# Kernel tuning notes

Hardware: AMD Instinct MI355X
Metric: run time of the kernel (lower is better)

Reference implementation:

```python
import jax, jax.numpy as jnp
import numpy as np

N = 50000      # nodes
E = 800000     # edges (avg degree 16)
IN = 512       # in_feats
HID = 64       # hidden_dim
HEADS = 4      # num_heads
NC = 40        # num_classes


def setup_inputs() -> dict:
    key = jax.random.key(0)
    ks = jax.random.split(key, 12)

    def p(k, shape, fan_in):
        return jax.random.normal(k, shape, jnp.float32) * (1.0 / np.sqrt(fan_in))

    x = jax.random.normal(ks[0], (N, IN), jnp.float32)
    edge_index = jax.random.randint(ks[1], (2, E), 0, N)
    return dict(
        x=x,
        edge_index=edge_index,
        W1=p(ks[2], (IN, HEADS * HID), IN),
        att_src1=p(ks[3], (HEADS, HID), HID),
        att_dst1=p(ks[4], (HEADS, HID), HID),
        b1=jnp.zeros((HEADS * HID,), jnp.float32),
        W2=p(ks[5], (HEADS * HID, HID), HEADS * HID),
        att_src2=p(ks[6], (1, HID), HID),
        att_dst2=p(ks[7], (1, HID), HID),
        b2=jnp.zeros((HID,), jnp.float32),
        mw1=p(ks[8], (HID, 64), HID),
        mb1=jnp.zeros((64,), jnp.float32),
        mw2=p(ks[9], (64, NC), 64),
        mb2=jnp.zeros((NC,), jnp.float32),
    )


def gat_layer(x, edge_index, W, att_src, att_dst, bias):
    # PyG GATConv with add_self_loops=False, concat=True, negative_slope=0.2
    H, C = att_src.shape
    n = x.shape[0]
    h = (x @ W).reshape(n, H, C)                       # [N,H,C]
    a_src = jnp.sum(h * att_src, axis=-1)              # [N,H]
    a_dst = jnp.sum(h * att_dst, axis=-1)              # [N,H]
    src, dst = edge_index[0], edge_index[1]
    e = jax.nn.leaky_relu(a_src[src] + a_dst[dst], 0.2)  # [E,H]
    # segment softmax grouped by destination node
    m = jax.ops.segment_max(e, dst, num_segments=n)
    ex = jnp.exp(e - m[dst])
    denom = jax.ops.segment_sum(ex, dst, num_segments=n)
    alpha = ex / (denom[dst] + 1e-16)                  # [E,H]
    out = jax.ops.segment_sum(h[src] * alpha[:, :, None], dst, num_segments=n)  # [N,H,C]
    return out.reshape(n, H * C) + bias


def reference(x, edge_index, W1, att_src1, att_dst1, b1,
              W2, att_src2, att_dst2, b2, mw1, mb1, mw2, mb2):
    h = jax.nn.elu(gat_layer(x, edge_index, W1, att_src1, att_dst1, b1))   # [N, HEADS*HID]
    emb = gat_layer(h, edge_index, W2, att_src2, att_dst2, b2)             # [N, HID] (heads=1)
    return jax.nn.relu(emb @ mw1 + mb1) @ mw2 + mb2                        # [N, NC]
```

## Files before the change

### kernel.cpp

```cpp
#include <hip/hip_runtime.h>

#define N_NODES 50000
#define N_EDGES 800000
#define SCAN_B 196

typedef short bf16x8 __attribute__((ext_vector_type(8)));
typedef float f32x4 __attribute__((ext_vector_type(4)));

__device__ __forceinline__ unsigned short f2bf_rne(float x) {
  unsigned u = __float_as_uint(x);
  u += 0x7FFFu + ((u >> 16) & 1u);
  return (unsigned short)(u >> 16);
}

__global__ __launch_bounds__(256) void hist_k(const int* __restrict__ ei,
                                              int* __restrict__ cnt) {
  int e = blockIdx.x * 256 + threadIdx.x;
  if (e >= N_EDGES) return;
  atomicAdd(&cnt[ei[N_EDGES + e]], 1);
}

__global__ __launch_bounds__(256) void scan1(const int* __restrict__ cnt,
                                             int* __restrict__ offs,
                                             int* __restrict__ bsum) {
  __shared__ int sh[256];
  int t = threadIdx.x;
  int i = blockIdx.x * 256 + t;
  int v = (i < N_NODES) ? cnt[i] : 0;
  sh[t] = v;
  __syncthreads();
  for (int off = 1; off < 256; off <<= 1) {
    int add = (t >= off) ? sh[t - off] : 0;
    __syncthreads();
    sh[t] += add;
    __syncthreads();
  }
  if (i < N_NODES) offs[i] = sh[t] - v;
  if (t == 255) bsum[blockIdx.x] = sh[255];
}

__global__ __launch_bounds__(256) void scan2(const int* __restrict__ bsum,
                                             int* __restrict__ bofs) {
  __shared__ int sh[256];
  int t = threadIdx.x;
  int v = (t < SCAN_B) ? bsum[t] : 0;
  sh[t] = v;
  __syncthreads();
  for (int off = 1; off < 256; off <<= 1) {
    int add = (t >= off) ? sh[t - off] : 0;
    __syncthreads();
    sh[t] += add;
    __syncthreads();
  }
  if (t < SCAN_B) bofs[t] = sh[t] - v;
}

__global__ __launch_bounds__(256) void scan3(int* __restrict__ offs,
                                             const int* __restrict__ bofs) {
  int i = blockIdx.x * 256 + threadIdx.x;
  if (i < N_NODES) offs[i] += bofs[blockIdx.x];
  if (i == 0) offs[N_NODES] = N_EDGES;
}

__global__ __launch_bounds__(256) void scatter_k(const int* __restrict__ ei,
                                                 const int* __restrict__ offs,
                                                 int* __restrict__ cur,
                                                 int* __restrict__ ssort) {
  int e = blockIdx.x * 256 + threadIdx.x;
  if (e >= N_EDGES) return;
  int d = ei[N_EDGES + e];
  int p = offs[d] + atomicAdd(&cur[d], 1);
  ssort[p] = ei[e];
}

__device__ __forceinline__ void split2(float x, short& hi, short& lo) {
  unsigned u = __float_as_uint(x);
  unsigned short h = (unsigned short)(u >> 16);
  float hf = __uint_as_float((unsigned)h << 16);
  float r = x - hf;
  unsigned short l = (unsigned short)(__float_as_uint(r) >> 16);
  hi = (short)h;
  lo = (short)l;
}

template <int BN, int WGM, int WGN>
__global__ __launch_bounds__(256) void gemm_mfma(
    const float* __restrict__ A, const float* __restrict__ B,
    float* __restrict__ C, unsigned short* __restrict__ Cb,
    int M, int Nn, int K) {
  constexpr int BM = 128;
  constexpr int WM = BM / WGM;
  constexpr int WN = BN / WGN;
  constexpr int MT = WM / 16;
  constexpr int NT = WN / 16;
  constexpr int LDA = 40;
  constexpr int KPER = BN / 8;

  __shared__ short Ah[BM][LDA], Al[BM][LDA];
  __shared__ short Bh[BN][LDA], Bl[BN][LDA];

  const int tid = threadIdx.x;
  const int wave = tid >> 6;
  const int lane = tid & 63;
  const int quad = lane >> 4;
  const int l16 = lane & 15;
  const int wm = (wave / WGN) * WM;
  const int wn = (wave % WGN) * WN;
  const int rowBase = blockIdx.x * BM;
  const int colBase = blockIdx.y * BN;

  const int ra = tid >> 1;
  const int apart = (tid & 1) * 16;
  const int nb = tid & (BN - 1);
  const int kb = (tid / BN) * KPER;

  const int arow = min(rowBase + ra, M - 1);
  const float* aptr = A + (size_t)arow * K + apart;

  f32x4 acc[MT][NT] = {};

  for (int k0 = 0; k0 < K; k0 += 32) {
    {
      alignas(16) short h[16], l[16];
      const float4* a4 = (const float4*)(aptr + k0);
#pragma unroll
      for (int i = 0; i < 4; ++i) {
        float4 v = a4[i];
        split2(v.x, h[i * 4 + 0], l[i * 4 + 0]);
        split2(v.y, h[i * 4 + 1], l[i * 4 + 1]);
        split2(v.z, h[i * 4 + 2], l[i * 4 + 2]);
        split2(v.w, h[i * 4 + 3], l[i * 4 + 3]);
      }
      *(bf16x8*)&Ah[ra][apart]     = ((bf16x8*)h)[0];
      *(bf16x8*)&Ah[ra][apart + 8] = ((bf16x8*)h)[1];
      *(bf16x8*)&Al[ra][apart]     = ((bf16x8*)l)[0];
      *(bf16x8*)&Al[ra][apart + 8] = ((bf16x8*)l)[1];
    }
    {
      alignas(16) short h[KPER], l[KPER];
#pragma unroll
      for (int i = 0; i < KPER; ++i) {
        float v = B[(size_t)(k0 + kb + i) * Nn + colBase + nb];
        split2(v, h[i], l[i]);
      }
#pragma unroll
      for (int i = 0; i < KPER / 8; ++i) {
        *(bf16x8*)&Bh[nb][kb + i * 8] = ((bf16x8*)h)[i];
        *(bf16x8*)&Bl[nb][kb + i * 8] = ((bf16x8*)l)[i];
      }
    }
    __syncthreads();
    bf16x8 afh[MT], afl[MT], bfh[NT], bfl[NT];
#pragma unroll
    for (int mt = 0; mt < MT; ++mt) {
      afh[mt] = *(const bf16x8*)&Ah[wm + mt * 16 + l16][quad * 8];
      afl[mt] = *(const bf16x8*)&Al[wm + mt * 16 + l16][quad * 8];
    }
#pragma unroll
    for (int nt = 0; nt < NT; ++nt) {
      bfh[nt] = *(const bf16x8*)&Bh[wn + nt * 16 + l16][quad * 8];
      bfl[nt] = *(const bf16x8*)&Bl[wn + nt * 16 + l16][quad * 8];
    }
#pragma unroll
    for (int mt = 0; mt < MT; ++mt)
#pragma unroll
      for (int nt = 0; nt < NT; ++nt) {
        acc[mt][nt] = __builtin_amdgcn_mfma_f32_16x16x32_bf16(afh[mt], bfh[nt], acc[mt][nt], 0, 0, 0);
        acc[mt][nt] = __builtin_amdgcn_mfma_f32_16x16x32_bf16(afh[mt], bfl[nt], acc[mt][nt], 0, 0, 0);
        acc[mt][nt] = __builtin_amdgcn_mfma_f32_16x16x32_bf16(afl[mt], bfh[nt], acc[mt][nt], 0, 0, 0);
      }
    __syncthreads();
  }
#pragma unroll
  for (int mt = 0; mt < MT; ++mt) {
    int r0 = rowBase + wm + mt * 16 + quad * 4;
#pragma unroll
    for (int nt = 0; nt < NT; ++nt) {
      int c = colBase + wn + nt * 16 + l16;
#pragma unroll
      for (int reg = 0; reg < 4; ++reg) {
        int r = r0 + reg;
        if (r < M) {
          float v = acc[mt][nt][reg];
          C[(size_t)r * Nn + c] = v;
          if (Cb) Cb[(size_t)r * Nn + c] = f2bf_rne(v);
        }
      }
    }
  }
}

__global__ __launch_bounds__(256) void attdot4(
    const float* __restrict__ h1, const float* __restrict__ att_src,
    const float* __restrict__ att_dst, float* __restrict__ a_src,
    float* __restrict__ a_dst, int n) {
  int node = blockIdx.x * 4 + (threadIdx.x >> 6);
  int lane = threadIdx.x & 63;
  if (node >= n) return;
  const float* hrow = h1 + (size_t)node * 256;
#pragma unroll
  for (int h = 0; h < 4; ++h) {
    float v = hrow[h * 64 + lane];
    float s = v * att_src[h * 64 + lane];
    float d = v * att_dst[h * 64 + lane];
#pragma unroll
    for (int off = 32; off > 0; off >>= 1) {
      s += __shfl_xor(s, off);
      d += __shfl_xor(d, off);
    }
    if (lane == 0) {
      a_src[node * 4 + h] = s;
      a_dst[node * 4 + h] = d;
    }
  }
}

__global__ __launch_bounds__(256) void attdot1h(
    const float* __restrict__ h2, const float* __restrict__ att_src,
    const float* __restrict__ att_dst, float* __restrict__ a_src,
    float* __restrict__ a_dst, int n) {
  int node = blockIdx.x * 4 + (threadIdx.x >> 6);
  int lane = threadIdx.x & 63;
  if (node >= n) return;
  float v = h2[(size_t)node * 64 + lane];
  float s = v * att_src[lane];
  float d = v * att_dst[lane];
#pragma unroll
  for (int off = 32; off > 0; off >>= 1) {
    s += __shfl_xor(s, off);
    d += __shfl_xor(d, off);
  }
  if (lane == 0) {
    a_src[node] = s;
    a_dst[node] = d;
  }
}

__global__ __launch_bounds__(128) void agg_l1(
    const int* __restrict__ offs, const int* __restrict__ ssort,
    const float* __restrict__ asrc, const float* __restrict__ adst,
    const unsigned short* __restrict__ h1b, const float* __restrict__ b1,
    float* __restrict__ outp) {
  const int d = blockIdx.x;
  const int t = threadIdx.x;
  const int h = t >> 5;
  __shared__ int s_src[128];
  __shared__ float s_ex[128 * 4];
  const int row0 = offs[d], row1 = offs[d + 1];
  const float4 ad4 = *(const float4*)&adst[d * 4];
  float acc0 = 0.f, acc1 = 0.f, denom = 0.f;

  for (int j0 = row0; j0 < row1; j0 += 128) {
    const int n = min(128, row1 - j0);
    if (t < n) {
      int s = ssort[j0 + t];
      s_src[t] = s;
      float4 as = *(const float4*)&asrc[s * 4];
      float4 sc;
      sc.x = as.x + ad4.x; sc.x = sc.x > 0.f ? sc.x : 0.2f * sc.x;
      sc.y = as.y + ad4.y; sc.y = sc.y > 0.f ? sc.y : 0.2f * sc.y;
      sc.z = as.z + ad4.z; sc.z = sc.z > 0.f ? sc.z : 0.2f * sc.z;
      sc.w = as.w + ad4.w; sc.w = sc.w > 0.f ? sc.w : 0.2f * sc.w;
      sc.x = __expf(sc.x); sc.y = __expf(sc.y);
      sc.z = __expf(sc.z); sc.w = __expf(sc.w);
      *(float4*)&s_ex[t * 4] = sc;
    }
    __syncthreads();
    for (int j = 0; j < n; ++j) {
      float exv = s_ex[j * 4 + h];
      unsigned pv = *(const unsigned*)&h1b[(size_t)s_src[j] * 256 + 2 * t];
      float f0 = __uint_as_float(pv << 16);
      float f1 = __uint_as_float(pv & 0xFFFF0000u);
      acc0 += f0 * exv;
      acc1 += f1 * exv;
      denom += exv;
    }
    __syncthreads();
  }
  float inv = denom > 0.f ? 1.f / denom : 0.f;
  float v0 = acc0 * inv + b1[2 * t];
  float v1 = acc1 * inv + b1[2 * t + 1];
  float2 r;
  r.x = v0 > 0.f ? v0 : expm1f(v0);
  r.y = v1 > 0.f ? v1 : expm1f(v1);
  *(float2*)&outp[(size_t)d * 256 + 2 * t] = r;
}

__global__ __launch_bounds__(256) void agg_l2(
    const int* __restrict__ offs, const int* __restrict__ ssort,
    const float* __restrict__ asrc, const float* __restrict__ adst,
    const unsigned short* __restrict__ h2b, const float* __restrict__ b2,
    float* __restrict__ outp, int n_nodes) {
  int d = blockIdx.x * 4 + (threadIdx.x >> 6);
  int lane = threadIdx.x & 63;
  if (d >= n_nodes) return;
  const int row0 = offs[d], row1 = offs[d + 1];
  const float ad = adst[d];
  float acc = 0.f, denom = 0.f;

  for (int j0 = row0; j0 < row1; j0 += 64) {
    const int n = min(64, row1 - j0);
    int s = 0;
    float ex = 0.f;
    if (lane < n) {
      s = ssort[j0 + lane];
      float sc = asrc[s] + ad;
      sc = sc > 0.f ? sc : 0.2f * sc;
      ex = __expf(sc);
    }
    float ds = ex;
#pragma unroll
    for (int off = 32; off > 0; off >>= 1) ds += __shfl_xor(ds, off);
    denom += ds;
    for (int j = 0; j < n; ++j) {
      int sj = __shfl(s, j);
      float exj = __shfl(ex, j);
      float f = __uint_as_float((unsigned)h2b[(size_t)sj * 64 + lane] << 16);
      acc += f * exj;
    }
  }
  float val = (denom > 0.f ? acc / denom : 0.f) + b2[lane];
  outp[(size_t)d * 64 + lane] = val;
}

__global__ __launch_bounds__(256) void mlp_head(
    const float* __restrict__ emb_in,
    const float* __restrict__ mw1, const float* __restrict__ mb1,
    const float* __restrict__ mw2, const float* __restrict__ mb2,
    float* __restrict__ outp, int n) {
  __shared__ float w1s[64 * 64];
  __shared__ float w2s[64 * 40];
  __shared__ float b1s[64];
  __shared__ float b2s[40];
  int t = threadIdx.x;
  for (int i = t; i < 64 * 64; i += 256) w1s[i] = mw1[i];
  for (int i = t; i < 64 * 40; i += 256) w2s[i] = mw2[i];
  if (t < 64) b1s[t] = mb1[t];
  if (t < 40) b2s[t] = mb2[t];
  __syncthreads();
  int node = blockIdx.x * 256 + t;
  if (node >= n) return;
  float emb[64];
#pragma unroll
  for (int i = 0; i < 64; ++i) emb[i] = emb_in[(size_t)node * 64 + i];
  float hid[64];
#pragma unroll
  for (int j = 0; j < 64; ++j) {
    float s = b1s[j];
#pragma unroll
    for (int i = 0; i < 64; ++i) s += emb[i] * w1s[i * 64 + j];
    hid[j] = s > 0.f ? s : 0.f;
  }
#pragma unroll
  for (int k = 0; k < 40; ++k) {
    float s = b2s[k];
#pragma unroll
    for (int j = 0; j < 64; ++j) s += hid[j] * w2s[j * 40 + k];
    outp[(size_t)node * 40 + k] = s;
  }
}

extern "C" void kernel_launch(void* const* d_in, const int* in_sizes, int n_in,
                              void* d_out, int out_size, void* d_ws, size_t ws_size,
                              hipStream_t stream) {
  const float* x        = (const float*)d_in[0];
  const int*   ei       = (const int*)d_in[1];
  const float* W1       = (const float*)d_in[2];
  const float* att_src1 = (const float*)d_in[3];
  const float* att_dst1 = (const float*)d_in[4];
  const float* b1       = (const float*)d_in[5];
  const float* W2       = (const float*)d_in[6];
  const float* att_src2 = (const float*)d_in[7];
  const float* att_dst2 = (const float*)d_in[8];
  const float* b2       = (const float*)d_in[9];
  const float* mw1      = (const float*)d_in[10];
  const float* mb1      = (const float*)d_in[11];
  const float* mw2      = (const float*)d_in[12];
  const float* mb2      = (const float*)d_in[13];
  float* out = (float*)d_out;

  const int N = N_NODES, E = N_EDGES;
  char* base = (char*)d_ws;
  size_t o = 0;
  auto alloc = [&](size_t n_elems) {
    void* p = base + o;
    o += n_elems * 4;
    return p;
  };
  int* cnt = (int*)alloc(N);
  int* cur = (int*)alloc(N);
  size_t zero_bytes = o;
  int*   offs  = (int*)alloc(N + 2);
  int*   bsum  = (int*)alloc(256);
  int*   bofs  = (int*)alloc(256);
  int*   ssort = (int*)alloc(E);
  float* h1    = (float*)alloc((size_t)N * 256);
  float* h1e   = (float*)alloc((size_t)N * 256);
  float* asrc1 = (float*)alloc((size_t)N * 4);
  float* adst1 = (float*)alloc((size_t)N * 4);
  float* h2    = (float*)alloc((size_t)N * 64);
  float* emb   = (float*)alloc((size_t)N * 64);
  float* asrc2 = (float*)alloc(N);
  float* adst2 = (float*)alloc(N);
  unsigned short* h1b = (unsigned short*)alloc((size_t)N * 128);
  unsigned short* h2b = (unsigned short*)alloc((size_t)N * 32);

  hipMemsetAsync(d_ws, 0, zero_bytes, stream);

  const int EB = (E + 255) / 256;

  hist_k<<<EB, 256, 0, stream>>>(ei, cnt);
  scan1<<<SCAN_B, 256, 0, stream>>>(cnt, offs, bsum);
  scan2<<<1, 256, 0, stream>>>(bsum, bofs);
  scan3<<<SCAN_B, 256, 0, stream>>>(offs, bofs);
  scatter_k<<<EB, 256, 0, stream>>>(ei, offs, cur, ssort);

  dim3 g1((N + 127) / 128, 256 / 128);
  gemm_mfma<128, 2, 2><<<g1, 256, 0, stream>>>(x, W1, h1, h1b, N, 256, 512);
  attdot4<<<(N + 3) / 4, 256, 0, stream>>>(h1, att_src1, att_dst1, asrc1, adst1, N);
  agg_l1<<<N, 128, 0, stream>>>(offs, ssort, asrc1, adst1, h1b, b1, h1e);

  dim3 g2((N + 127) / 128, 1);
  gemm_mfma<64, 4, 1><<<g2, 256, 0, stream>>>(h1e, W2, h2, h2b, N, 64, 256);
  attdot1h<<<(N + 3) / 4, 256, 0, stream>>>(h2, att_src2, att_dst2, asrc2, adst2, N);
  agg_l2<<<(N + 3) / 4, 256, 0, stream>>>(offs, ssort, asrc2, adst2, h2b, b2, emb, N);

  mlp_head<<<(N + 255) / 256, 256, 0, stream>>>(emb, mw1, mb1, mw2, mb2, out, N);
}
```

Measured before the change: 562.5 us.

## Fuse attention dot products into GEMM epilogues and pre-split weights to bf16

Weights are split into bf16 hi/lo once by a small kernel laid out in K-groups of 8, then streamed into LDS with global_load_lds instead of being split per block inside the GEMM loop. Both GEMMs now compute the attention source/destination dot products in their epilogue via lane shuffles and LDS, which removes the separate attdot kernels and the fp32 h1/h2 writes and reads. Each layer avoids a large fp32 intermediate write and reread. In exchange it adds two small extra launches and depends on the direct-to-LDS load path and the new B layout being correct.

```diff
diff --git a/kernel.cpp b/kernel.cpp
--- a/kernel.cpp
+++ b/kernel.cpp
@@ -6,11 +6,26 @@
 
 typedef short bf16x8 __attribute__((ext_vector_type(8)));
 typedef float f32x4 __attribute__((ext_vector_type(4)));
+
+#define GLDS16(g, l)                                                  \
+  __builtin_amdgcn_global_load_lds(                                   \
+      (const __attribute__((address_space(1))) void*)(g),             \
+      (__attribute__((address_space(3))) void*)(l), 16, 0, 0)
 
 __device__ __forceinline__ unsigned short f2bf_rne(float x) {
   unsigned u = __float_as_uint(x);
   u += 0x7FFFu + ((u >> 16) & 1u);
   return (unsigned short)(u >> 16);
+}
+
+__device__ __forceinline__ void split2(float x, short& hi, short& lo) {
+  unsigned u = __float_as_uint(x);
+  unsigned short h = (unsigned short)(u >> 16);
+  float hf = __uint_as_float((unsigned)h << 16);
+  float r = x - hf;
+  unsigned short l = (unsigned short)(__float_as_uint(r) >> 16);
+  hi = (short)h;
+  lo = (short)l;
 }
 
 __global__ __launch_bounds__(256) void hist_k(const int* __restrict__ ei,
@@ -73,56 +88,62 @@
   ssort[p] = ei[e];
 }
 
-__device__ __forceinline__ void split2(float x, short& hi, short& lo) {
-  unsigned u = __float_as_uint(x);
-  unsigned short h = (unsigned short)(u >> 16);
-  float hf = __uint_as_float((unsigned)h << 16);
-  float r = x - hf;
-  unsigned short l = (unsigned short)(__float_as_uint(r) >> 16);
-  hi = (short)h;
-  lo = (short)l;
-}
-
-template <int BN, int WGM, int WGN>
-__global__ __launch_bounds__(256) void gemm_mfma(
-    const float* __restrict__ A, const float* __restrict__ B,
-    float* __restrict__ C, unsigned short* __restrict__ Cb,
-    int M, int Nn, int K) {
-  constexpr int BM = 128;
-  constexpr int WM = BM / WGM;
-  constexpr int WN = BN / WGN;
-  constexpr int MT = WM / 16;
-  constexpr int NT = WN / 16;
+__global__ __launch_bounds__(256) void wsplit(
+    const float* __restrict__ W, unsigned short* __restrict__ Wh,
+    unsigned short* __restrict__ Wl, int K, int Nn) {
+  int i = blockIdx.x * 256 + threadIdx.x;
+  int total = (K >> 3) * Nn;
+  if (i >= total) return;
+  int kq = i / Nn;
+  int n = i % Nn;
+  alignas(16) short h[8], l[8];
+#pragma unroll
+  for (int j = 0; j < 8; ++j) {
+    float v = W[(size_t)(kq * 8 + j) * Nn + n];
+    split2(v, h[j], l[j]);
+  }
+  size_t dst = (size_t)i * 8;
+  *(bf16x8*)&Wh[dst] = *(bf16x8*)h;
+  *(bf16x8*)&Wl[dst] = *(bf16x8*)l;
+}
+
+__global__ __launch_bounds__(256) void gemm1_fused(
+    const float* __restrict__ A,
+    const unsigned short* __restrict__ Bh_g, const unsigned short* __restrict__ Bl_g,
+    const float* __restrict__ att_s, const float* __restrict__ att_d,
+    unsigned short* __restrict__ h1b, float* __restrict__ asrc,
+    float* __restrict__ adst, int M) {
+  constexpr int K = 512, Nn = 256;
   constexpr int LDA = 40;
-  constexpr int KPER = BN / 8;
-
-  __shared__ short Ah[BM][LDA], Al[BM][LDA];
-  __shared__ short Bh[BN][LDA], Bl[BN][LDA];
+  __shared__ short Ah[128][LDA], Al[128][LDA];
+  __shared__ short Bh[4 * 128 * 8], Bl[4 * 128 * 8];
+  __shared__ float attLds[128][4];
 
   const int tid = threadIdx.x;
-  const int wave = tid >> 6;
-  const int lane = tid & 63;
-  const int quad = lane >> 4;
-  const int l16 = lane & 15;
-  const int wm = (wave / WGN) * WM;
-  const int wn = (wave % WGN) * WN;
-  const int rowBase = blockIdx.x * BM;
-  const int colBase = blockIdx.y * BN;
-
-  const int ra = tid >> 1;
-  const int apart = (tid & 1) * 16;
-  const int nb = tid & (BN - 1);
-  const int kb = (tid / BN) * KPER;
-
+  const int wave = tid >> 6, lane = tid & 63;
+  const int quad = lane >> 4, l16 = lane & 15;
+  const int wm = (wave >> 1) * 64, wn = (wave & 1) * 64;
+  const int rowBase = blockIdx.x * 128;
+  const int colBase = blockIdx.y * 128;
+
+  const int ra = tid >> 1, apart = (tid & 1) * 16;
   const int arow = min(rowBase + ra, M - 1);
   const float* aptr = A + (size_t)arow * K + apart;
 
-  f32x4 acc[MT][NT] = {};
-
-  for (int k0 = 0; k0 < K; k0 += 32) {
+  f32x4 acc[4][4] = {};
+
+  for (int kc = 0; kc < K / 32; ++kc) {
+#pragma unroll
+    for (int inst = 0; inst < 2; ++inst) {
+      int seq = inst * 256 + tid;
+      int gq = seq >> 7, nl = seq & 127;
+      size_t gsrc = (((size_t)kc * 4 + gq) * Nn + colBase + nl) * 8;
+      GLDS16(Bh_g + gsrc, &Bh[seq * 8]);
+      GLDS16(Bl_g + gsrc, &Bl[seq * 8]);
+    }
     {
       alignas(16) short h[16], l[16];
-      const float4* a4 = (const float4*)(aptr + k0);
+      const float4* a4 = (const float4*)(aptr + kc * 32);
 #pragma unroll
       for (int i = 0; i < 4; ++i) {
         float4 v = a4[i];
@@ -136,103 +157,190 @@
       *(bf16x8*)&Al[ra][apart]     = ((bf16x8*)l)[0];
       *(bf16x8*)&Al[ra][apart + 8] = ((bf16x8*)l)[1];
     }
-    {
-      alignas(16) short h[KPER], l[KPER];
-#pragma unroll
-      for (int i = 0; i < KPER; ++i) {
-        float v = B[(size_t)(k0 + kb + i) * Nn + colBase + nb];
-        split2(v, h[i], l[i]);
-      }
-#pragma unroll
-      for (int i = 0; i < KPER / 8; ++i) {
-        *(bf16x8*)&Bh[nb][kb + i * 8] = ((bf16x8*)h)[i];
-        *(bf16x8*)&Bl[nb][kb + i * 8] = ((bf16x8*)l)[i];
-      }
-    }
-    __syncthreads();
-    bf16x8 afh[MT], afl[MT], bfh[NT], bfl[NT];
-#pragma unroll
-    for (int mt = 0; mt < MT; ++mt) {
+    __syncthreads();
+    bf16x8 afh[4], afl[4], bfh[4], bfl[4];
+#pragma unroll
+    for (int mt = 0; mt < 4; ++mt) {
       afh[mt] = *(const bf16x8*)&Ah[wm + mt * 16 + l16][quad * 8];
       afl[mt] = *(const bf16x8*)&Al[wm + mt * 16 + l16][quad * 8];
     }
 #pragma unroll
-    for (int nt = 0; nt < NT; ++nt) {
-      bfh[nt] = *(const bf16x8*)&Bh[wn + nt * 16 + l16][quad * 8];
-      bfl[nt] = *(const bf16x8*)&Bl[wn + nt * 16 + l16][quad * 8];
-    }
-#pragma unroll
-    for (int mt = 0; mt < MT; ++mt)
-#pragma unroll
-      for (int nt = 0; nt < NT; ++nt) {
+    for (int nt = 0; nt < 4; ++nt) {
+      int bi = ((quad << 7) + wn + nt * 16 + l16) * 8;
+      bfh[nt] = *(const bf16x8*)&Bh[bi];
+      bfl[nt] = *(const bf16x8*)&Bl[bi];
+    }
+#pragma unroll
+    for (int mt = 0; mt < 4; ++mt)
+#pragma unroll
+      for (int nt = 0; nt < 4; ++nt) {
         acc[mt][nt] = __builtin_amdgcn_mfma_f32_16x16x32_bf16(afh[mt], bfh[nt], acc[mt][nt], 0, 0, 0);
         acc[mt][nt] = __builtin_amdgcn_mfma_f32_16x16x32_bf16(afh[mt], bfl[nt], acc[mt][nt], 0, 0, 0);
         acc[mt][nt] = __builtin_amdgcn_mfma_f32_16x16x32_bf16(afl[mt], bfh[nt], acc[mt][nt], 0, 0, 0);
       }
     __syncthreads();
   }
-#pragma unroll
-  for (int mt = 0; mt < MT; ++mt) {
-    int r0 = rowBase + wm + mt * 16 + quad * 4;
-#pragma unroll
-    for (int nt = 0; nt < NT; ++nt) {
-      int c = colBase + wn + nt * 16 + l16;
-#pragma unroll
-      for (int reg = 0; reg < 4; ++reg) {
-        int r = r0 + reg;
+
+  float asw[4], adw[4];
+#pragma unroll
+  for (int nt = 0; nt < 4; ++nt) {
+    int c = colBase + wn + nt * 16 + l16;
+    asw[nt] = att_s[c];
+    adw[nt] = att_d[c];
+  }
+#pragma unroll
+  for (int mt = 0; mt < 4; ++mt) {
+    int rl = wm + mt * 16 + quad * 4;
+#pragma unroll
+    for (int reg = 0; reg < 4; ++reg) {
+      int r = rowBase + rl + reg;
+      float s = 0.f, dd = 0.f;
+#pragma unroll
+      for (int nt = 0; nt < 4; ++nt) {
+        float v = acc[mt][nt][reg];
+        s += v * asw[nt];
+        dd += v * adw[nt];
         if (r < M) {
-          float v = acc[mt][nt][reg];
-          C[(size_t)r * Nn + c] = v;
-          if (Cb) Cb[(size_t)r * Nn + c] = f2bf_rne(v);
+          int c = colBase + wn + nt * 16 + l16;
+          h1b[(size_t)r * Nn + c] = f2bf_rne(v);
         }
       }
-    }
-  }
-}
-
-__global__ __launch_bounds__(256) void attdot4(
-    const float* __restrict__ h1, const float* __restrict__ att_src,
-    const float* __restrict__ att_dst, float* __restrict__ a_src,
-    float* __restrict__ a_dst, int n) {
-  int node = blockIdx.x * 4 + (threadIdx.x >> 6);
-  int lane = threadIdx.x & 63;
-  if (node >= n) return;
-  const float* hrow = h1 + (size_t)node * 256;
-#pragma unroll
-  for (int h = 0; h < 4; ++h) {
-    float v = hrow[h * 64 + lane];
-    float s = v * att_src[h * 64 + lane];
-    float d = v * att_dst[h * 64 + lane];
-#pragma unroll
-    for (int off = 32; off > 0; off >>= 1) {
-      s += __shfl_xor(s, off);
-      d += __shfl_xor(d, off);
-    }
-    if (lane == 0) {
-      a_src[node * 4 + h] = s;
-      a_dst[node * 4 + h] = d;
-    }
-  }
-}
-
-__global__ __launch_bounds__(256) void attdot1h(
-    const float* __restrict__ h2, const float* __restrict__ att_src,
-    const float* __restrict__ att_dst, float* __restrict__ a_src,
-    float* __restrict__ a_dst, int n) {
-  int node = blockIdx.x * 4 + (threadIdx.x >> 6);
-  int lane = threadIdx.x & 63;
-  if (node >= n) return;
-  float v = h2[(size_t)node * 64 + lane];
-  float s = v * att_src[lane];
-  float d = v * att_dst[lane];
-#pragma unroll
-  for (int off = 32; off > 0; off >>= 1) {
-    s += __shfl_xor(s, off);
-    d += __shfl_xor(d, off);
-  }
-  if (lane == 0) {
-    a_src[node] = s;
-    a_dst[node] = d;
+#pragma unroll
+      for (int off = 1; off < 16; off <<= 1) {
+        s += __shfl_xor(s, off);
+        dd += __shfl_xor(dd, off);
+      }
+      if (l16 == 0) {
+        attLds[rl + reg][(wn >> 6) * 2 + 0] = s;
+        attLds[rl + reg][(wn >> 6) * 2 + 1] = dd;
+      }
+    }
+  }
+  __syncthreads();
+  if (tid < 128) {
+    int r = rowBase + tid;
+    if (r < M) {
+      int hb = colBase >> 6;
+      asrc[r * 4 + hb + 0] = attLds[tid][0];
+      adst[r * 4 + hb + 0] = attLds[tid][1];
+      asrc[r * 4 + hb + 1] = attLds[tid][2];
+      adst[r * 4 + hb + 1] = attLds[tid][3];
+    }
+  }
+}
+
+__global__ __launch_bounds__(256) void gemm2_fused(
+    const float* __restrict__ A,
+    const unsigned short* __restrict__ Bh_g, const unsigned short* __restrict__ Bl_g,
+    const float* __restrict__ att_s, const float* __restrict__ att_d,
+    unsigned short* __restrict__ h2b, float* __restrict__ asrc,
+    float* __restrict__ adst, int M) {
+  constexpr int K = 256, Nn = 64;
+  constexpr int LDA = 40;
+  __shared__ short Ah[128][LDA], Al[128][LDA];
+  __shared__ short Bh[4 * 64 * 8], Bl[4 * 64 * 8];
+  __shared__ float attLds[128][2];
+
+  const int tid = threadIdx.x;
+  const int wave = tid >> 6, lane = tid & 63;
+  const int quad = lane >> 4, l16 = lane & 15;
+  const int wm = wave * 32;
+  const int rowBase = blockIdx.x * 128;
+
+  const int ra = tid >> 1, apart = (tid & 1) * 16;
+  const int arow = min(rowBase + ra, M - 1);
+  const float* aptr = A + (size_t)arow * K + apart;
+
+  f32x4 acc[2][4] = {};
+
+  for (int kc = 0; kc < K / 32; ++kc) {
+    {
+      size_t gsrc = (((size_t)kc * 4) * Nn) * 8 + (size_t)tid * 8;
+      GLDS16(Bh_g + gsrc, &Bh[tid * 8]);
+      GLDS16(Bl_g + gsrc, &Bl[tid * 8]);
+    }
+    {
+      alignas(16) short h[16], l[16];
+      const float4* a4 = (const float4*)(aptr + kc * 32);
+#pragma unroll
+      for (int i = 0; i < 4; ++i) {
+        float4 v = a4[i];
+        split2(v.x, h[i * 4 + 0], l[i * 4 + 0]);
+        split2(v.y, h[i * 4 + 1], l[i * 4 + 1]);
+        split2(v.z, h[i * 4 + 2], l[i * 4 + 2]);
+        split2(v.w, h[i * 4 + 3], l[i * 4 + 3]);
+      }
+      *(bf16x8*)&Ah[ra][apart]     = ((bf16x8*)h)[0];
+      *(bf16x8*)&Ah[ra][apart + 8] = ((bf16x8*)h)[1];
+      *(bf16x8*)&Al[ra][apart]     = ((bf16x8*)l)[0];
+      *(bf16x8*)&Al[ra][apart + 8] = ((bf16x8*)l)[1];
+    }
+    __syncthreads();
+    bf16x8 afh[2], afl[2], bfh[4], bfl[4];
+#pragma unroll
+    for (int mt = 0; mt < 2; ++mt) {
+      afh[mt] = *(const bf16x8*)&Ah[wm + mt * 16 + l16][quad * 8];
+      afl[mt] = *(const bf16x8*)&Al[wm + mt * 16 + l16][quad * 8];
+    }
+#pragma unroll
+    for (int nt = 0; nt < 4; ++nt) {
+      int bi = ((quad << 6) + nt * 16 + l16) * 8;
+      bfh[nt] = *(const bf16x8*)&Bh[bi];
+      bfl[nt] = *(const bf16x8*)&Bl[bi];
+    }
+#pragma unroll
+    for (int mt = 0; mt < 2; ++mt)
+#pragma unroll
+      for (int nt = 0; nt < 4; ++nt) {
+        acc[mt][nt] = __builtin_amdgcn_mfma_f32_16x16x32_bf16(afh[mt], bfh[nt], acc[mt][nt], 0, 0, 0);
+        acc[mt][nt] = __builtin_amdgcn_mfma_f32_16x16x32_bf16(afh[mt], bfl[nt], acc[mt][nt], 0, 0, 0);
+        acc[mt][nt] = __builtin_amdgcn_mfma_f32_16x16x32_bf16(afl[mt], bfh[nt], acc[mt][nt], 0, 0, 0);
+      }
+    __syncthreads();
+  }
+
+  float asw[4], adw[4];
+#pragma unroll
+  for (int nt = 0; nt < 4; ++nt) {
+    int c = nt * 16 + l16;
+    asw[nt] = att_s[c];
+    adw[nt] = att_d[c];
+  }
+#pragma unroll
+  for (int mt = 0; mt < 2; ++mt) {
+    int rl = wm + mt * 16 + quad * 4;
+#pragma unroll
+    for (int reg = 0; reg < 4; ++reg) {
+      int r = rowBase + rl + reg;
+      float s = 0.f, dd = 0.f;
+#pragma unroll
+      for (int nt = 0; nt < 4; ++nt) {
+        float v = acc[mt][nt][reg];
+        s += v * asw[nt];
+        dd += v * adw[nt];
+        if (r < M) {
+          int c = nt * 16 + l16;
+          h2b[(size_t)r * Nn + c] = f2bf_rne(v);
+        }
+      }
+#pragma unroll
+      for (int off = 1; off < 16; off <<= 1) {
+        s += __shfl_xor(s, off);
+        dd += __shfl_xor(dd, off);
+      }
+      if (l16 == 0) {
+        attLds[rl + reg][0] = s;
+        attLds[rl + reg][1] = dd;
+      }
+    }
+  }
+  __syncthreads();
+  if (tid < 128) {
+    int r = rowBase + tid;
+    if (r < M) {
+      asrc[r] = attLds[tid][0];
+      adst[r] = attLds[tid][1];
+    }
   }
 }
 
@@ -394,16 +502,18 @@
   int*   bsum  = (int*)alloc(256);
   int*   bofs  = (int*)alloc(256);
   int*   ssort = (int*)alloc(E);
-  float* h1    = (float*)alloc((size_t)N * 256);
   float* h1e   = (float*)alloc((size_t)N * 256);
   float* asrc1 = (float*)alloc((size_t)N * 4);
   float* adst1 = (float*)alloc((size_t)N * 4);
-  float* h2    = (float*)alloc((size_t)N * 64);
   float* emb   = (float*)alloc((size_t)N * 64);
   float* asrc2 = (float*)alloc(N);
   float* adst2 = (float*)alloc(N);
   unsigned short* h1b = (unsigned short*)alloc((size_t)N * 128);
   unsigned short* h2b = (unsigned short*)alloc((size_t)N * 32);
+  unsigned short* w1h = (unsigned short*)alloc(512 * 256 / 2);
+  unsigned short* w1l = (unsigned short*)alloc(512 * 256 / 2);
+  unsigned short* w2h = (unsigned short*)alloc(256 * 64 / 2);
+  unsigned short* w2l = (unsigned short*)alloc(256 * 64 / 2);
 
   hipMemsetAsync(d_ws, 0, zero_bytes, stream);
 
@@ -414,15 +524,17 @@
   scan2<<<1, 256, 0, stream>>>(bsum, bofs);
   scan3<<<SCAN_B, 256, 0, stream>>>(offs, bofs);
   scatter_k<<<EB, 256, 0, stream>>>(ei, offs, cur, ssort);
-
-  dim3 g1((N + 127) / 128, 256 / 128);
-  gemm_mfma<128, 2, 2><<<g1, 256, 0, stream>>>(x, W1, h1, h1b, N, 256, 512);
-  attdot4<<<(N + 3) / 4, 256, 0, stream>>>(h1, att_src1, att_dst1, asrc1, adst1, N);
+  wsplit<<<(512 / 8 * 256 + 255) / 256, 256, 0, stream>>>(W1, w1h, w1l, 512, 256);
+  wsplit<<<(256 / 8 * 64 + 255) / 256, 256, 0, stream>>>(W2, w2h, w2l, 256, 64);
+
+  dim3 g1((N + 127) / 128, 2);
+  gemm1_fused<<<g1, 256, 0, stream>>>(x, w1h, w1l, att_src1, att_dst1,
+                                      h1b, asrc1, adst1, N);
   agg_l1<<<N, 128, 0, stream>>>(offs, ssort, asrc1, adst1, h1b, b1, h1e);
 
   dim3 g2((N + 127) / 128, 1);
-  gemm_mfma<64, 4, 1><<<g2, 256, 0, stream>>>(h1e, W2, h2, h2b, N, 64, 256);
-  attdot1h<<<(N + 3) / 4, 256, 0, stream>>>(h2, att_src2, att_dst2, asrc2, adst2, N);
+  gemm2_fused<<<g2, 256, 0, stream>>>(h1e, w2h, w2l, att_src2, att_dst2,
+                                      h2b, asrc2, adst2, N);
   agg_l2<<<(N + 3) / 4, 256, 0, stream>>>(offs, ssort, asrc2, adst2, h2b, b2, emb, N);
 
   mlp_head<<<(N + 255) / 256, 256, 0, stream>>>(emb, mw1, mb1, mw2, mb2, out, N);
```

Result: faster. 512.0 us (-9.0%).
